# Kernel optimization log

Hardware: AMD Instinct MI355X
Metric: run time of the kernel (lower is better)

The kernel has to match this reference:

```python
import jax, jax.numpy as jnp
from jax import lax
import numpy as np

THRESHOLD = 1.25
CURRENT_DECAY = 0.25
VOLTAGE_DECAY = 0.03
TAU_GRAD = 0.03
SCALE_GRAD = 3.0


@jax.custom_vjp
def spike_fn(v):
    # Heaviside spike on membrane voltage (threshold already subtracted)
    return (v >= 0.0).astype(v.dtype)

def _spike_fwd(v):
    return spike_fn(v), v

def _spike_bwd(v, g):
    # slayer-style exponential surrogate gradient around threshold
    surrogate = SCALE_GRAD * jnp.exp(-jnp.abs(v) / TAU_GRAD)
    return (g * surrogate,)

spike_fn.defvjp(_spike_fwd, _spike_bwd)


def cuba_dense(x, v_w, g_w, delay):
    """x: [B, C_in, T] spikes -> [B, C_out, T] spikes.
    Weight-normalized dense synapse + CUBA leaky-integrate-and-fire scan + axonal delay."""
    # weight norm: W = g * v / ||v||_row
    norm = jnp.sqrt(jnp.sum(v_w * v_w, axis=1, keepdims=True))
    W = g_w[:, None] * v_w / norm                       # [O, C]
    z = jnp.einsum('bct,oc->bot', x, W)                 # synaptic current input [B, O, T]
    B, O, T = z.shape
    zT = jnp.transpose(z, (2, 0, 1))                    # [T, B, O]

    def step(carry, zt):
        cur, vol = carry
        cur = cur * (1.0 - CURRENT_DECAY) + zt
        vol = vol * (1.0 - VOLTAGE_DECAY) + cur
        s = spike_fn(vol - THRESHOLD)
        vol = vol * (1.0 - s)                           # reset to zero on spike
        return (cur, vol), s

    init = (jnp.zeros((B, O), z.dtype), jnp.zeros((B, O), z.dtype))
    _, sT = lax.scan(step, init, zT)                    # [T, B, O]
    s = jnp.transpose(sT, (1, 2, 0))                    # [B, O, T]

    # per-neuron integer axonal delay: out[b,n,t] = s[b,n,t-d_n]
    t_idx = jnp.arange(T)[None, :] - delay[:, None]     # [O, T]
    valid = (t_idx >= 0)
    gathered = s[:, jnp.arange(O)[:, None], jnp.clip(t_idx, 0, T - 1)]
    return jnp.where(valid[None, :, :], gathered, jnp.zeros((), s.dtype))


def setup_inputs() -> dict:
    key = jax.random.key(0)
    ks = jax.random.split(key, 10)
    B, C, T = 32, 34 * 34 * 2, 300
    spike = (jax.random.uniform(ks[0], (B, C, T)) < 0.1).astype(jnp.float32)
    v1 = jax.random.normal(ks[1], (512, C), jnp.float32) * 0.1
    g1 = jax.random.uniform(ks[2], (512,), jnp.float32) + 0.5
    v2 = jax.random.normal(ks[3], (512, 512), jnp.float32) * 0.1
    g2 = jax.random.uniform(ks[4], (512,), jnp.float32) + 0.5
    v3 = jax.random.normal(ks[5], (10, 512), jnp.float32) * 0.1
    g3 = jax.random.uniform(ks[6], (10,), jnp.float32) + 0.5
    d1 = jax.random.randint(ks[7], (512,), 0, 8, jnp.int32)
    d2 = jax.random.randint(ks[8], (512,), 0, 8, jnp.int32)
    d3 = jax.random.randint(ks[9], (10,), 0, 8, jnp.int32)
    return {"spike": spike, "v1": v1, "g1": g1, "v2": v2, "g2": g2,
            "v3": v3, "g3": g3, "d1": d1, "d2": d2, "d3": d3}


def reference(spike, v1, g1, v2, g2, v3, g3, d1, d2, d3):
    s1 = cuba_dense(spike, v1, g1, d1)
    s2 = cuba_dense(s1, v2, g2, d2)
    s3 = cuba_dense(s2, v3, g3, d3)
    counts = jnp.stack([jnp.mean(s1), jnp.mean(s2), jnp.mean(s3)]).reshape(1, -1)
    return s3, counts
```

## Files before the change

### kernel.cpp

```cpp
#include <hip/hip_runtime.h>

#define B_   32
#define T_   300
#define C1_  2312
#define O1_  512
#define O2_  512
#define O3_  10
#define M_   (B_*T_)
#define KSPLIT_ 1152


__global__ void calc_f(const float* __restrict__ v, const float* __restrict__ g,
                       double* __restrict__ f, int O, int C) {
    int o = blockIdx.x;
    const float* row = v + (size_t)o * C;
    double s = 0.0;
    for (int c = threadIdx.x; c < C; c += blockDim.x) {
        double x = (double)row[c];
        s += x * x;
    }
    for (int off = 32; off; off >>= 1) s += __shfl_down(s, off);
    __shared__ double wsum[4];
    int lane = threadIdx.x & 63, wv = threadIdx.x >> 6;
    if (lane == 0) wsum[wv] = s;
    __syncthreads();
    if (threadIdx.x == 0) {
        double tot = 0.0;
        for (int i = 0; i < (int)(blockDim.x >> 6); ++i) tot += wsum[i];
        f[o] = (double)g[o] / sqrt(tot);
    }
}

__global__ void transpose_scale(const float* __restrict__ v, const double* __restrict__ f,
                                double* __restrict__ wt, int O, int C, int ldo) {
    __shared__ double tile[32][33];
    int c0 = blockIdx.x * 32, o0 = blockIdx.y * 32;
    int tx = threadIdx.x, ty = threadIdx.y;
    for (int k = 0; k < 4; ++k) {
        int o = o0 + ty + k * 8, c = c0 + tx;
        double val = 0.0;
        if (o < O && c < C) val = (double)v[(size_t)o * C + c] * f[o];
        tile[ty + k * 8][tx] = val;
    }
    __syncthreads();
    for (int k = 0; k < 4; ++k) {
        int c = c0 + ty + k * 8, o = o0 + tx;
        if (c < C && o < O) wt[(size_t)c * ldo + o] = tile[tx][ty + k * 8];
    }
}

__global__ void build_bits(const float* __restrict__ X, unsigned* __restrict__ bits) {
    size_t idx = (size_t)blockIdx.x * 256 + threadIdx.x;
    if (idx >= (size_t)B_ * C1_ * 10) return;
    int t32 = (int)(idx % 10);
    size_t bc = idx / 10;
    const float* src = X + bc * T_ + t32 * 32;
    int nq = (t32 == 9) ? 3 : 8;
    unsigned m = 0;
    for (int q = 0; q < nq; ++q) {
        float4 v = *(const float4*)(src + q * 4);
        if (v.x != 0.f) m |= 1u << (q * 4 + 0);
        if (v.y != 0.f) m |= 1u << (q * 4 + 1);
        if (v.z != 0.f) m |= 1u << (q * 4 + 2);
        if (v.w != 0.f) m |= 1u << (q * 4 + 3);
    }
    bits[idx] = m;
}

__global__ __launch_bounds__(512, 4) void gemm1(const unsigned* __restrict__ Xbits,
                                                const double* __restrict__ Wt,
                                                double* __restrict__ Z0,
                                                double* __restrict__ Z1) {
    __shared__ double Ws[2][16][256];
    int n = blockIdx.x;
    int combo = n & 3;
    int khalf = combo & 1;
    int o0 = (combo >> 1) * 256;
    int i = n >> 2;
    int tb = i % 10;
    int bpair = i / 10;
    int tid = threadIdx.x;
    int w = tid >> 6;
    int lane = tid & 63;
    int b = bpair * 2 + (w >> 2);
    int w8s = __builtin_amdgcn_readfirstlane((w & 3) << 3);
    int cbeg = khalf ? KSPLIT_ : 0;
    int qend = khalf ? C1_ : KSPLIT_;
    const int NT = khalf ? 73 : 72;
    double* __restrict__ Z = khalf ? Z1 : Z0;
    double acc[8][4];
#pragma unroll
    for (int tj = 0; tj < 8; ++tj)
#pragma unroll
        for (int i2 = 0; i2 < 4; ++i2) acc[tj][i2] = 0.0;
    const unsigned* xbp = Xbits + (size_t)b * C1_ * 10 + tb;

    double2 wreg[4];
    unsigned mval, mvaln = 0u;

    auto load_w = [&](int c0) {
#pragma unroll
        for (int h = 0; h < 4; ++h) {
            int idx = h * 512 + tid;
            int r = idx >> 7, od = (idx & 127) * 2;
            int c = c0 + r;
            double2 val; val.x = 0.0; val.y = 0.0;
            if (c < qend) val = *(const double2*)(Wt + (size_t)c * O1_ + o0 + od);
            wreg[h] = val;
        }
    };
    auto load_m = [&](int c0) -> unsigned {
        int c = c0 + lane;
        return (lane < 16 && c < qend) ? xbp[(size_t)c * 10] : 0u;
    };
    auto store_w = [&](int bi) {
#pragma unroll
        for (int h = 0; h < 4; ++h) {
            int idx = h * 512 + tid;
            int r = idx >> 7, od = (idx & 127) * 2;
            *(double2*)(&Ws[bi][r][od]) = wreg[h];
        }
    };

    load_w(cbeg);
    mval = load_m(cbeg);
    store_w(0);
    __syncthreads();
    int cur = 0;
    for (int tile = 0; tile < NT; ++tile) {
        if (tile + 1 < NT) {
            int cn = cbeg + (tile + 1) * 16;
            load_w(cn);
            mvaln = load_m(cn);
        }
#pragma unroll
        for (int k = 0; k < 16; ++k) {
            unsigned smk = (unsigned)__builtin_amdgcn_readlane((int)mval, k);
            unsigned soct = (smk >> w8s) & 0xffu;
            if (soct) {
                double wf[4];
#pragma unroll
                for (int i2 = 0; i2 < 4; ++i2) wf[i2] = Ws[cur][k][lane + 64 * i2];
#pragma unroll
                for (int tj = 0; tj < 8; ++tj) {
                    if (soct & (1u << tj)) {
#pragma unroll
                        for (int i2 = 0; i2 < 4; ++i2) acc[tj][i2] += wf[i2];
                    }
                }
            }
        }
        if (tile + 1 < NT) {
            store_w(cur ^ 1);
            __syncthreads();
        }
        mval = mvaln;
        cur ^= 1;
    }
#pragma unroll
    for (int tj = 0; tj < 8; ++tj) {
        int t = tb * 32 + w8s + tj;
        if (t < T_) {
            double* dst = Z + ((size_t)b * T_ + t) * O1_ + o0;
#pragma unroll
            for (int i2 = 0; i2 < 4; ++i2)
                dst[lane + 64 * i2] = acc[tj][i2];
        }
    }
}

__global__ __launch_bounds__(256, 4) void gemm2(const float* __restrict__ A,
                                                const double* __restrict__ Wt,
                                                double* __restrict__ Z) {
    __shared__ double Ws[16][128];
    __shared__ float  As[32][20];
    int m0 = blockIdx.x * 32;
    int o0 = blockIdx.y * 128;
    int tid = threadIdx.x;
    int to = tid & 31, tm = tid >> 5;
    double acc[4][4];
#pragma unroll
    for (int i = 0; i < 4; ++i)
#pragma unroll
        for (int j = 0; j < 4; ++j) acc[i][j] = 0.0;
    for (int c0 = 0; c0 < 512; c0 += 16) {
        {
            int r = tid >> 3, pr = tid & 7;
            float2 v = *(const float2*)(A + (size_t)(m0 + r) * 512 + c0 + pr * 2);
            As[r][pr * 2 + 0] = v.x;
            As[r][pr * 2 + 1] = v.y;
        }
#pragma unroll
        for (int h = 0; h < 4; ++h) {
            int idx = h * 512 + tid * 2;
            int k = idx >> 7, o = idx & 127;
            *(double2*)(&Ws[k][o]) = *(const double2*)(Wt + (size_t)(c0 + k) * O2_ + o0 + o);
        }
        __syncthreads();
#pragma unroll
        for (int k = 0; k < 16; ++k) {
            double wf[4], xf[4];
#pragma unroll
            for (int i = 0; i < 4; ++i) wf[i] = Ws[k][to + 32 * i];
#pragma unroll
            for (int j = 0; j < 4; ++j) xf[j] = (double)As[tm * 4 + j][k];
#pragma unroll
            for (int i = 0; i < 4; ++i)
#pragma unroll
                for (int j = 0; j < 4; ++j) acc[i][j] = fma(wf[i], xf[j], acc[i][j]);
        }
        __syncthreads();
    }
#pragma unroll
    for (int j = 0; j < 4; ++j) {
        double* dst = Z + (size_t)(m0 + tm * 4 + j) * O2_ + o0;
#pragma unroll
        for (int i = 0; i < 4; ++i) dst[to + 32 * i] = acc[i][j];
    }
}

__global__ void gemm3(const float* __restrict__ A,
                      const double* __restrict__ Wt,
                      double* __restrict__ Z) {
    __shared__ double w[512 * 16];
    for (int e = threadIdx.x; e < 4096; e += 256)
        ((double2*)w)[e] = ((const double2*)Wt)[e];
    __syncthreads();
    int m = blockIdx.x * 256 + threadIdx.x;
    if (m >= M_) return;
    double acc[O3_];
#pragma unroll
    for (int o = 0; o < O3_; ++o) acc[o] = 0.0;
    const float4* Ar = (const float4*)(A + (size_t)m * 512);
    for (int cq = 0; cq < 128; ++cq) {
        float4 a = Ar[cq];
        float av[4] = {a.x, a.y, a.z, a.w};
#pragma unroll
        for (int u = 0; u < 4; ++u)
#pragma unroll
            for (int o = 0; o < O3_; ++o) acc[o] += (double)av[u] * w[(cq * 4 + u) * 16 + o];
    }
    double* dst = Z + (size_t)m * 16;
#pragma unroll
    for (int o = 0; o < O3_; ++o) dst[o] = acc[o];
}

__global__ void scan12(const double* __restrict__ Za,
                       const double* __restrict__ Zb,
                       const int* __restrict__ delay,
                       float* __restrict__ Sout,
                       unsigned* __restrict__ bitsOut,
                       float* __restrict__ sumOut) {
    int blk = blockIdx.x;
    int o = (blk & 7) * 64 + threadIdx.x;
    int b = blk >> 3;
    size_t base = (size_t)b * T_ * O1_ + o;
    const double* z  = Za + base;
    const double* z2 = Zb ? Zb + base : nullptr;
    float* s = Sout ? Sout + base : nullptr;
    int d = delay[o];
    if (s) for (int t = 0; t < d; ++t) s[(size_t)t * O1_] = 0.f;
    double cur = 0.0, vol = 0.0;
    float cnt = 0.f;
    unsigned bw = 0u;
    for (int t8 = 0; t8 < 296; t8 += 8) {
        double zbuf[8];
#pragma unroll
        for (int u = 0; u < 8; ++u) zbuf[u] = z[(size_t)(t8 + u) * O1_];
        if (z2) {
#pragma unroll
            for (int u = 0; u < 8; ++u) zbuf[u] += z2[(size_t)(t8 + u) * O1_];
        }
#pragma unroll
        for (int u = 0; u < 8; ++u) {
            int t = t8 + u;
            cur = cur * 0.75 + zbuf[u];
            vol = vol * 0.97 + cur;
            float sp = (vol >= 1.25) ? 1.f : 0.f;
            if (sp > 0.f) vol = 0.0;
            int tw = t + d;
            if (tw < T_) {
                if (s) s[(size_t)tw * O1_] = sp;
                cnt += sp;
                if (bitsOut) {
                    if (sp > 0.f) bw |= 1u << (tw & 31);
                    if ((tw & 31) == 31) { bitsOut[((size_t)b * O1_ + o) * 10 + (tw >> 5)] = bw; bw = 0u; }
                }
            }
        }
    }
    {
        double zbuf[4];
#pragma unroll
        for (int u = 0; u < 4; ++u) zbuf[u] = z[(size_t)(296 + u) * O1_];
        if (z2) {
#pragma unroll
            for (int u = 0; u < 4; ++u) zbuf[u] += z2[(size_t)(296 + u) * O1_];
        }
#pragma unroll
        for (int u = 0; u < 4; ++u) {
            int t = 296 + u;
            cur = cur * 0.75 + zbuf[u];
            vol = vol * 0.97 + cur;
            float sp = (vol >= 1.25) ? 1.f : 0.f;
            if (sp > 0.f) vol = 0.0;
            int tw = t + d;
            if (tw < T_) {
                if (s) s[(size_t)tw * O1_] = sp;
                cnt += sp;
                if (bitsOut) {
                    if (sp > 0.f) bw |= 1u << (tw & 31);
                    if ((tw & 31) == 31) { bitsOut[((size_t)b * O1_ + o) * 10 + (tw >> 5)] = bw; bw = 0u; }
                }
            }
        }
    }
    if (bitsOut) bitsOut[((size_t)b * O1_ + o) * 10 + 9] = bw;
    for (int off = 32; off; off >>= 1) cnt += __shfl_down(cnt, off);
    if (threadIdx.x == 0) atomicAdd(sumOut, cnt);
}

__global__ void scan3(const double* __restrict__ Z3,
                      const int* __restrict__ d3,
                      float* __restrict__ out,
                      float* __restrict__ sumOut) {
    __shared__ double zt[T_ * 16];
    int b = blockIdx.x;
    const double2* src = (const double2*)(Z3 + (size_t)b * T_ * 16);
    for (int e = threadIdx.x; e < T_ * 8; e += 64)
        ((double2*)zt)[e] = src[e];
    __syncthreads();
    int o = threadIdx.x;
    if (o < O3_) {
        int d = d3[o];
        float* dst = out + (size_t)b * O3_ * T_ + (size_t)o * T_;
        for (int t = 0; t < d; ++t) dst[t] = 0.f;
        double cur = 0.0, vol = 0.0;
        float cnt = 0.f;
        for (int t = 0; t < T_; ++t) {
            cur = cur * 0.75 + zt[t * 16 + o];
            vol = vol * 0.97 + cur;
            float sp = (vol >= 1.25) ? 1.f : 0.f;
            if (sp > 0.f) vol = 0.0;
            int tw = t + d;
            if (tw < T_) { dst[tw] = sp; cnt += sp; }
        }
        atomicAdd(sumOut, cnt);
    }
}

__global__ void finalize(const float* __restrict__ sums, float* __restrict__ out) {
    if (threadIdx.x == 0) {
        out[0] = (float)((double)sums[0] / (double)(B_ * O1_ * T_));
        out[1] = (float)((double)sums[1] / (double)(B_ * O2_ * T_));
        out[2] = (float)((double)sums[2] / (double)(B_ * O3_ * T_));
    }
}

extern "C" void kernel_launch(void* const* d_in, const int* in_sizes, int n_in,
                              void* d_out, int out_size, void* d_ws, size_t ws_size,
                              hipStream_t stream) {
    const float* spike = (const float*)d_in[0];
    const float* v1 = (const float*)d_in[1];
    const float* g1 = (const float*)d_in[2];
    const float* v2 = (const float*)d_in[3];
    const float* g2 = (const float*)d_in[4];
    const float* v3 = (const float*)d_in[5];
    const float* g3 = (const float*)d_in[6];
    const int* d1 = (const int*)d_in[7];
    const int* d2 = (const int*)d_in[8];
    const int* d3 = (const int*)d_in[9];
    float* out = (float*)d_out;

    double* dw = (double*)d_ws;
    size_t off = 0;
    double* f1  = dw + off; off += 512;
    double* f2  = dw + off; off += 512;
    double* f3  = dw + off; off += 16;
    double* Wt1 = dw + off; off += (size_t)C1_ * O1_;
    double* Wt2 = dw + off; off += 512 * 512;
    double* Wt3 = dw + off; off += 512 * 16;
    double* zA  = dw + off; off += (size_t)M_ * 512;
    double* zB  = dw + off; off += (size_t)M_ * 512;
    double* z3b = dw + off; off += (size_t)M_ * 16;
    float* fw = (float*)(dw + off);
    float* sB    = fw;
    float* sums  = fw + (size_t)M_ * 512;
    unsigned* Xbits = (unsigned*)(fw + (size_t)M_ * 512 + 4);
    (void)ws_size; (void)out_size; (void)in_sizes; (void)n_in;

    hipMemsetAsync(sums, 0, 4 * sizeof(float), stream);

    build_bits<<<(B_ * C1_ * 10 + 255) / 256, 256, 0, stream>>>(spike, Xbits);

    calc_f<<<512, 256, 0, stream>>>(v1, g1, f1, O1_, C1_);
    calc_f<<<512, 256, 0, stream>>>(v2, g2, f2, O2_, O1_);
    calc_f<<<O3_, 256, 0, stream>>>(v3, g3, f3, O3_, O2_);

    transpose_scale<<<dim3((C1_ + 31) / 32, 16), dim3(32, 8), 0, stream>>>(v1, f1, Wt1, O1_, C1_, O1_);
    transpose_scale<<<dim3(16, 16), dim3(32, 8), 0, stream>>>(v2, f2, Wt2, O2_, O1_, O2_);
    transpose_scale<<<dim3(16, 1), dim3(32, 8), 0, stream>>>(v3, f3, Wt3, O3_, O2_, 16);

    gemm1<<<640, 512, 0, stream>>>(Xbits, Wt1, zA, zB);
    scan12<<<256, 64, 0, stream>>>(zA, zB, d1, sB, nullptr, sums + 0);
    gemm2<<<dim3(300, 4), 256, 0, stream>>>(sB, Wt2, zA);
    scan12<<<256, 64, 0, stream>>>(zA, nullptr, d2, sB, nullptr, sums + 1);
    gemm3<<<(M_ + 255) / 256, 256, 0, stream>>>(sB, Wt3, z3b);
    scan3<<<B_, 64, 0, stream>>>(z3b, d3, out, sums + 2);
    finalize<<<1, 64, 0, stream>>>(sums, out + (size_t)B_ * O3_ * T_);
}
```

Before: 794.9 us.

## Enlarge gemm2 tile with double-buffered LDS and split gemm1 into templated halves

gemm2 now computes a 64x128 tile per block, giving each thread 8x4 accumulators, and double-buffers the weight and activation tiles through registers so the next k-slice loads while the current one computes. The aim is more FLOPs per LDS/global byte and less time stalled on barriers. gemm1 is split into two templated launches, one per K half, so the K-range branches become compile-time constants. The larger gemm2 tile increases register pressure, which forces occupancy down to 3 blocks, and launches half as many blocks.

```diff
diff --git a/kernel.cpp b/kernel.cpp
--- a/kernel.cpp
+++ b/kernel.cpp
@@ -67,16 +67,15 @@
     bits[idx] = m;
 }
 
-__global__ __launch_bounds__(512, 4) void gemm1(const unsigned* __restrict__ Xbits,
-                                                const double* __restrict__ Wt,
-                                                double* __restrict__ Z0,
-                                                double* __restrict__ Z1) {
+template<int KH>
+__global__ __launch_bounds__(512, 4) void gemm1h(const unsigned* __restrict__ Xbits,
+                                                 const double* __restrict__ Wt,
+                                                 double* __restrict__ Z) {
     __shared__ double Ws[2][16][256];
     int n = blockIdx.x;
-    int combo = n & 3;
-    int khalf = combo & 1;
-    int o0 = (combo >> 1) * 256;
-    int i = n >> 2;
+    int ohalf = n & 1;
+    int o0 = ohalf * 256;
+    int i = n >> 1;
     int tb = i % 10;
     int bpair = i / 10;
     int tid = threadIdx.x;
@@ -84,10 +83,9 @@
     int lane = tid & 63;
     int b = bpair * 2 + (w >> 2);
     int w8s = __builtin_amdgcn_readfirstlane((w & 3) << 3);
-    int cbeg = khalf ? KSPLIT_ : 0;
-    int qend = khalf ? C1_ : KSPLIT_;
-    const int NT = khalf ? 73 : 72;
-    double* __restrict__ Z = khalf ? Z1 : Z0;
+    const int cbeg = KH ? KSPLIT_ : 0;
+    const int qend = KH ? C1_ : KSPLIT_;
+    const int NT = KH ? 73 : 72;
     double acc[8][4];
 #pragma unroll
     for (int tj = 0; tj < 8; ++tj)
@@ -169,53 +167,79 @@
     }
 }
 
-__global__ __launch_bounds__(256, 4) void gemm2(const float* __restrict__ A,
+__global__ __launch_bounds__(256, 3) void gemm2(const float* __restrict__ A,
                                                 const double* __restrict__ Wt,
                                                 double* __restrict__ Z) {
-    __shared__ double Ws[16][128];
-    __shared__ float  As[32][20];
-    int m0 = blockIdx.x * 32;
+    __shared__ double Ws[2][16][128];
+    __shared__ float  As[2][64][17];
+    int m0 = blockIdx.x * 64;
     int o0 = blockIdx.y * 128;
     int tid = threadIdx.x;
-    int to = tid & 31, tm = tid >> 5;
-    double acc[4][4];
-#pragma unroll
-    for (int i = 0; i < 4; ++i)
+    int to = tid & 15, tm = tid >> 4;
+    double acc[8][4];
+#pragma unroll
+    for (int i = 0; i < 8; ++i)
 #pragma unroll
         for (int j = 0; j < 4; ++j) acc[i][j] = 0.0;
-    for (int c0 = 0; c0 < 512; c0 += 16) {
-        {
-            int r = tid >> 3, pr = tid & 7;
-            float2 v = *(const float2*)(A + (size_t)(m0 + r) * 512 + c0 + pr * 2);
-            As[r][pr * 2 + 0] = v.x;
-            As[r][pr * 2 + 1] = v.y;
-        }
+
+    double2 wreg[4];
+    float4  areg;
+
+    auto load_regs = [&](int c0) {
 #pragma unroll
         for (int h = 0; h < 4; ++h) {
             int idx = h * 512 + tid * 2;
             int k = idx >> 7, o = idx & 127;
-            *(double2*)(&Ws[k][o]) = *(const double2*)(Wt + (size_t)(c0 + k) * O2_ + o0 + o);
-        }
-        __syncthreads();
+            wreg[h] = *(const double2*)(Wt + (size_t)(c0 + k) * O2_ + o0 + o);
+        }
+        {
+            int r = tid >> 2, ch = (tid & 3) * 4;
+            areg = *(const float4*)(A + (size_t)(m0 + r) * 512 + c0 + ch);
+        }
+    };
+    auto store_regs = [&](int bi) {
+#pragma unroll
+        for (int h = 0; h < 4; ++h) {
+            int idx = h * 512 + tid * 2;
+            int k = idx >> 7, o = idx & 127;
+            *(double2*)(&Ws[bi][k][o]) = wreg[h];
+        }
+        {
+            int r = tid >> 2, ch = (tid & 3) * 4;
+            As[bi][r][ch + 0] = areg.x; As[bi][r][ch + 1] = areg.y;
+            As[bi][r][ch + 2] = areg.z; As[bi][r][ch + 3] = areg.w;
+        }
+    };
+
+    load_regs(0);
+    store_regs(0);
+    __syncthreads();
+    int cur = 0;
+    for (int tile = 0; tile < 32; ++tile) {
+        if (tile + 1 < 32) load_regs((tile + 1) * 16);
 #pragma unroll
         for (int k = 0; k < 16; ++k) {
-            double wf[4], xf[4];
-#pragma unroll
-            for (int i = 0; i < 4; ++i) wf[i] = Ws[k][to + 32 * i];
-#pragma unroll
-            for (int j = 0; j < 4; ++j) xf[j] = (double)As[tm * 4 + j][k];
-#pragma unroll
-            for (int i = 0; i < 4; ++i)
+            double wf[8], xf[4];
+#pragma unroll
+            for (int i = 0; i < 8; ++i) wf[i] = Ws[cur][k][to + 16 * i];
+#pragma unroll
+            for (int j = 0; j < 4; ++j) xf[j] = (double)As[cur][tm * 4 + j][k];
+#pragma unroll
+            for (int i = 0; i < 8; ++i)
 #pragma unroll
                 for (int j = 0; j < 4; ++j) acc[i][j] = fma(wf[i], xf[j], acc[i][j]);
         }
-        __syncthreads();
+        if (tile + 1 < 32) {
+            store_regs(cur ^ 1);
+            __syncthreads();
+        }
+        cur ^= 1;
     }
 #pragma unroll
     for (int j = 0; j < 4; ++j) {
         double* dst = Z + (size_t)(m0 + tm * 4 + j) * O2_ + o0;
 #pragma unroll
-        for (int i = 0; i < 4; ++i) dst[to + 32 * i] = acc[i][j];
+        for (int i = 0; i < 8; ++i) dst[to + 16 * i] = acc[i][j];
     }
 }
 
@@ -401,9 +425,10 @@
     transpose_scale<<<dim3(16, 16), dim3(32, 8), 0, stream>>>(v2, f2, Wt2, O2_, O1_, O2_);
     transpose_scale<<<dim3(16, 1), dim3(32, 8), 0, stream>>>(v3, f3, Wt3, O3_, O2_, 16);
 
-    gemm1<<<640, 512, 0, stream>>>(Xbits, Wt1, zA, zB);
+    gemm1h<0><<<320, 512, 0, stream>>>(Xbits, Wt1, zA);
+    gemm1h<1><<<320, 512, 0, stream>>>(Xbits, Wt1, zB);
     scan12<<<256, 64, 0, stream>>>(zA, zB, d1, sB, nullptr, sums + 0);
-    gemm2<<<dim3(300, 4), 256, 0, stream>>>(sB, Wt2, zA);
+    gemm2<<<dim3(150, 4), 256, 0, stream>>>(sB, Wt2, zA);
     scan12<<<256, 64, 0, stream>>>(zA, nullptr, d2, sB, nullptr, sums + 1);
     gemm3<<<(M_ + 255) / 256, 256, 0, stream>>>(sB, Wt3, z3b);
     scan3<<<B_, 64, 0, stream>>>(z3b, d3, out, sums + 2);
```

Result: slower. 2.969 ms (+273.5%).
